# Kernel optimization log

Hardware: AMD Instinct MI355X
Metric: run time of the kernel (lower is better)

## Reference

```python
import jax, jax.numpy as jnp
import numpy as np

N_NODES = 10000
DEG = 32          # random neighbors per node; +1 self loop (A + I in original)
BATCH = 2
F_IN = 128
D_EMB = 128


def _make_edges():
    # np.where on a dense (A+I) matrix yields edges sorted by source row;
    # we build the same sorted-by-src edge list directly.
    rng = np.random.default_rng(0)
    src = np.repeat(np.arange(N_NODES), DEG + 1)
    dst = rng.integers(0, N_NODES, size=N_NODES * (DEG + 1))
    dst[DEG::DEG + 1] = np.arange(N_NODES)  # guarantee self loops
    return np.stack([src, dst], axis=1).astype(np.int32)  # [E, 2]


def setup_inputs() -> dict:
    key = jax.random.key(0)
    k1, k2, k3 = jax.random.split(key, 3)
    inputs = jax.random.normal(k1, (BATCH, N_NODES, F_IN), jnp.float32)
    W = jax.random.normal(k2, (F_IN, D_EMB), jnp.float32) * 0.1
    W_attn = jax.random.normal(k3, (2 * D_EMB, 1), jnp.float32) * 0.1
    edges = jnp.asarray(_make_edges())
    return {"inputs": inputs, "W": W, "W_attn": W_attn, "edges": edges}


def reference(inputs, W, W_attn, edges):
    # inputs: [B, N, F]; W: [F, D]; W_attn: [2D, 1]; edges: [E, 2] (sorted by src)
    B, N, _ = inputs.shape
    D = W.shape[1]
    src, dst = edges[:, 0], edges[:, 1]

    h = inputs @ W  # [B, N, D] node_states_transformed

    # Original: gather [src,dst] feats, reshape to [B,E,2D], matmul W_attn.
    # Equivalent efficient form: split W_attn and project per node first.
    a_src, a_dst = W_attn[:D, 0], W_attn[D:, 0]
    s = h @ a_src  # [B, N]
    d = h @ a_dst  # [B, N]
    scores = jax.nn.leaky_relu(s[:, src] + d[:, dst], negative_slope=0.2)  # [B, E]
    scores = jnp.exp(jnp.clip(scores, -2.0, 2.0))

    # Faithful to original bug: denominator uses batch 0 only, shared across batch.
    denom = jax.ops.segment_sum(scores[0], src, num_segments=N)  # [N]
    # edges sorted by src => tf.repeat(denom, bincount(src)) == denom[src]
    attn = scores / denom[src][None, :]  # [B, E]

    msgs = h[:, dst] * attn[:, :, None]  # [B, E, D]
    # tf.unsorted_segment_sum with rank-2 segment_ids sums over batch AND edges.
    out = jax.ops.segment_sum(msgs.sum(axis=0), src, num_segments=N)  # [N, D]
    return jnp.broadcast_to(out[None], (B, N, D))
```

## Files before the change

kernel.cpp:

```cpp
#include <hip/hip_runtime.h>
#include <math.h>

#define N_NODES 10000
#define DEG1 33
#define D_EMB 128
#define F_IN 128
#define BATCH 2

typedef short s8v  __attribute__((ext_vector_type(8)));
typedef float f4v  __attribute__((ext_vector_type(4)));

static __device__ __forceinline__ unsigned short f2bf(float f) {
    unsigned int x = __float_as_uint(f);
    unsigned int r = (x + 0x7fffu + ((x >> 16) & 1u)) >> 16;
    return (unsigned short)r;
}
static __device__ __forceinline__ float bf_lo(unsigned int u) { return __uint_as_float(u << 16); }
static __device__ __forceinline__ float bf_hi(unsigned int u) { return __uint_as_float(u & 0xffff0000u); }

__global__ __launch_bounds__(256) void gat_prep_kernel(
    const float* __restrict__ W, unsigned short* __restrict__ wtf)
{
    const int c = blockIdx.x;
    const int t = threadIdx.x;
    __shared__ float xs[128 * 16];
    #pragma unroll
    for (int r = 0; r < 8; ++r) {
        const int k = r * 16 + (t >> 4);
        const int n = t & 15;
        xs[k * 16 + n] = W[k * 128 + c * 16 + n];
    }
    __syncthreads();
    const int s = t >> 6;
    const int l = t & 63;
    s8v frag;
    #pragma unroll
    for (int j = 0; j < 8; ++j) {
        const int k = s * 32 + (l >> 4) * 8 + j;
        frag[j] = (short)f2bf(xs[k * 16 + (l & 15)]);
    }
    *(s8v*)&wtf[(((size_t)c * 4 + s) * 64 + l) * 8] = frag;
}

__global__ __launch_bounds__(256) void gat_h_kernel(
    const float* __restrict__ X, const unsigned short* __restrict__ wtf,
    const float* __restrict__ Wattn,
    unsigned short* __restrict__ hb, float* __restrict__ s_arr, float* __restrict__ d_arr)
{
    const int w = blockIdx.x * 4 + (threadIdx.x >> 6);
    if (w >= (BATCH * N_NODES) / 16) return;
    const int lane = threadIdx.x & 63;
    const int quad = lane >> 4;
    const int mrow = lane & 15;
    const int row0 = w * 16;

    f4v acc[8];
    #pragma unroll
    for (int c = 0; c < 8; ++c) acc[c] = (f4v){0.f, 0.f, 0.f, 0.f};

    const float* xrow = X + (size_t)(row0 + mrow) * F_IN;
    #pragma unroll
    for (int s = 0; s < 4; ++s) {
        const int k0 = s * 32 + quad * 8;
        const float4 xa = *(const float4*)&xrow[k0];
        const float4 xbv = *(const float4*)&xrow[k0 + 4];
        s8v a;
        a[0] = (short)f2bf(xa.x);  a[1] = (short)f2bf(xa.y);
        a[2] = (short)f2bf(xa.z);  a[3] = (short)f2bf(xa.w);
        a[4] = (short)f2bf(xbv.x); a[5] = (short)f2bf(xbv.y);
        a[6] = (short)f2bf(xbv.z); a[7] = (short)f2bf(xbv.w);
        #pragma unroll
        for (int c = 0; c < 8; ++c) {
            const s8v b = *(const s8v*)&wtf[(((size_t)c * 4 + s) * 64 + lane) * 8];
            acc[c] = __builtin_amdgcn_mfma_f32_16x16x32_bf16(a, b, acc[c], 0, 0, 0);
        }
    }

    const int b = (row0 >= N_NODES) ? 1 : 0;
    #pragma unroll
    for (int r = 0; r < 4; ++r) {
        const int R = row0 + quad * 4 + r;
        const int n = R - b * N_NODES;
        unsigned short* dst = &hb[((size_t)n * 2 + b) * D_EMB + mrow];
        #pragma unroll
        for (int c = 0; c < 8; ++c)
            dst[c * 16] = f2bf(acc[c][r]);
    }

    float as[8], ad[8];
    #pragma unroll
    for (int c = 0; c < 8; ++c) {
        as[c] = Wattn[c * 16 + mrow];
        ad[c] = Wattn[D_EMB + c * 16 + mrow];
    }
    #pragma unroll
    for (int r = 0; r < 4; ++r) {
        float sv = 0.f, dv = 0.f;
        #pragma unroll
        for (int c = 0; c < 8; ++c) {
            sv = fmaf(acc[c][r], as[c], sv);
            dv = fmaf(acc[c][r], ad[c], dv);
        }
        #pragma unroll
        for (int off = 1; off < 16; off <<= 1) {
            sv += __shfl_xor(sv, off, 16);
            dv += __shfl_xor(dv, off, 16);
        }
        if (mrow == 0) {
            const int R = row0 + quad * 4 + r;
            s_arr[R] = sv;
            d_arr[R] = dv;
        }
    }
}

__global__ __launch_bounds__(128) void gat_agg_kernel(
    const unsigned int* __restrict__ hb32, const float* __restrict__ s_arr,
    const float* __restrict__ d_arr, const int* __restrict__ edges,
    float* __restrict__ out)
{
    const int i = blockIdx.x;
    const int t = threadIdx.x;
    const int b = t >> 6;
    const int lane = t & 63;

    __shared__ int dsts[DEG1];
    __shared__ float scs[2][DEG1];
    __shared__ float inv_denom;
    __shared__ float red[2][2 * 64];

    float v = 0.f;
    if (lane < DEG1) {
        const int dst = edges[((size_t)i * DEG1 + lane) * 2 + 1];
        const float x0 = s_arr[b * N_NODES + i] + d_arr[b * N_NODES + dst];
        float x = (x0 >= 0.f) ? x0 : 0.2f * x0;
        x = fminf(fmaxf(x, -2.f), 2.f);
        const float sc = __expf(x);
        scs[b][lane] = sc;
        if (b == 0) { dsts[lane] = dst; v = sc; }
    }
    #pragma unroll
    for (int off = 32; off > 0; off >>= 1) v += __shfl_down(v, off, 64);
    if (t == 0) inv_denom = 1.f / v;
    __syncthreads();

    float ax = 0.f, ay = 0.f;
    #pragma unroll
    for (int j = 0; j < DEG1; ++j) {
        const int dd = dsts[j];
        const float wgt = scs[b][j];
        const unsigned int hv = hb32[((size_t)dd * 2 + b) * (D_EMB / 2) + lane];
        ax = fmaf(wgt, bf_lo(hv), ax);
        ay = fmaf(wgt, bf_hi(hv), ay);
    }
    red[b][2 * lane] = ax;
    red[b][2 * lane + 1] = ay;
    __syncthreads();

    const float inv = inv_denom;
    float2 o;
    o.x = (red[0][2 * lane] + red[1][2 * lane]) * inv;
    o.y = (red[0][2 * lane + 1] + red[1][2 * lane + 1]) * inv;
    *(float2*)&out[((size_t)b * N_NODES + i) * D_EMB + 2 * lane] = o;
}

extern "C" void kernel_launch(void* const* d_in, const int* in_sizes, int n_in,
                              void* d_out, int out_size, void* d_ws, size_t ws_size,
                              hipStream_t stream) {
    const float* X     = (const float*)d_in[0];
    const float* W     = (const float*)d_in[1];
    const float* Wattn = (const float*)d_in[2];
    const int*   edges = (const int*)d_in[3];
    float* out = (float*)d_out;

    unsigned short* wtf = (unsigned short*)d_ws;
    unsigned short* hb  = wtf + 16384;
    float* s_arr = (float*)(hb + (size_t)BATCH * N_NODES * D_EMB);
    float* d_arr = s_arr + BATCH * N_NODES;

    gat_prep_kernel<<<8, 256, 0, stream>>>(W, wtf);
    gat_h_kernel<<<313, 256, 0, stream>>>(X, wtf, Wattn, hb, s_arr, d_arr);
    gat_agg_kernel<<<N_NODES, 128, 0, stream>>>((const unsigned int*)hb, s_arr, d_arr, edges, out);
}
```

Before: 93.23 us.

## Split h GEMM columns across wave pairs and process nodes per wave in aggregation

The h projection kernel now gives each pair of waves one 16-row tile, with each wave computing half of the output columns. The partial attention dot products are combined through shared memory, which doubles the number of blocks for better occupancy. The aggregation kernel now gives one 64-lane wave per node and loops over 4 nodes per wave. It broadcasts neighbor indices and scores with shuffles instead of LDS and barriers, and gathers both batches with 8-byte loads. This removes per-node block launch and sync overhead, but each wave has less parallelism per node and the gathers are serialized across a longer per-wave loop.

```diff
diff --git a/kernel.cpp b/kernel.cpp
--- a/kernel.cpp
+++ b/kernel.cpp
@@ -47,16 +47,18 @@
     const float* __restrict__ Wattn,
     unsigned short* __restrict__ hb, float* __restrict__ s_arr, float* __restrict__ d_arr)
 {
-    const int w = blockIdx.x * 4 + (threadIdx.x >> 6);
-    if (w >= (BATCH * N_NODES) / 16) return;
+    __shared__ float lds_sd[2][2][2][16];
+    const int wave = threadIdx.x >> 6;
     const int lane = threadIdx.x & 63;
     const int quad = lane >> 4;
     const int mrow = lane & 15;
-    const int row0 = w * 16;
+    const int rg   = wave >> 1;
+    const int half = wave & 1;
+    const int row0 = (blockIdx.x * 2 + rg) * 16;
 
-    f4v acc[8];
+    f4v acc[4];
     #pragma unroll
-    for (int c = 0; c < 8; ++c) acc[c] = (f4v){0.f, 0.f, 0.f, 0.f};
+    for (int cc = 0; cc < 4; ++cc) acc[cc] = (f4v){0.f, 0.f, 0.f, 0.f};
 
     const float* xrow = X + (size_t)(row0 + mrow) * F_IN;
     #pragma unroll
@@ -70,9 +72,10 @@
         a[4] = (short)f2bf(xbv.x); a[5] = (short)f2bf(xbv.y);
         a[6] = (short)f2bf(xbv.z); a[7] = (short)f2bf(xbv.w);
         #pragma unroll
-        for (int c = 0; c < 8; ++c) {
+        for (int cc = 0; cc < 4; ++cc) {
+            const int c = half * 4 + cc;
             const s8v b = *(const s8v*)&wtf[(((size_t)c * 4 + s) * 64 + lane) * 8];
-            acc[c] = __builtin_amdgcn_mfma_f32_16x16x32_bf16(a, b, acc[c], 0, 0, 0);
+            acc[cc] = __builtin_amdgcn_mfma_f32_16x16x32_bf16(a, b, acc[cc], 0, 0, 0);
         }
     }
 
@@ -81,25 +84,25 @@
     for (int r = 0; r < 4; ++r) {
         const int R = row0 + quad * 4 + r;
         const int n = R - b * N_NODES;
-        unsigned short* dst = &hb[((size_t)n * 2 + b) * D_EMB + mrow];
+        unsigned short* dst = &hb[((size_t)n * 2 + b) * D_EMB + half * 64 + mrow];
         #pragma unroll
-        for (int c = 0; c < 8; ++c)
-            dst[c * 16] = f2bf(acc[c][r]);
+        for (int cc = 0; cc < 4; ++cc)
+            dst[cc * 16] = f2bf(acc[cc][r]);
     }
 
-    float as[8], ad[8];
+    float as[4], ad[4];
     #pragma unroll
-    for (int c = 0; c < 8; ++c) {
-        as[c] = Wattn[c * 16 + mrow];
-        ad[c] = Wattn[D_EMB + c * 16 + mrow];
+    for (int cc = 0; cc < 4; ++cc) {
+        as[cc] = Wattn[(half * 4 + cc) * 16 + mrow];
+        ad[cc] = Wattn[D_EMB + (half * 4 + cc) * 16 + mrow];
     }
     #pragma unroll
     for (int r = 0; r < 4; ++r) {
         float sv = 0.f, dv = 0.f;
         #pragma unroll
-        for (int c = 0; c < 8; ++c) {
-            sv = fmaf(acc[c][r], as[c], sv);
-            dv = fmaf(acc[c][r], ad[c], dv);
+        for (int cc = 0; cc < 4; ++cc) {
+            sv = fmaf(acc[cc][r], as[cc], sv);
+            dv = fmaf(acc[cc][r], ad[cc], dv);
         }
         #pragma unroll
         for (int off = 1; off < 16; off <<= 1) {
@@ -107,61 +110,72 @@
             dv += __shfl_xor(dv, off, 16);
         }
         if (mrow == 0) {
-            const int R = row0 + quad * 4 + r;
-            s_arr[R] = sv;
-            d_arr[R] = dv;
+            lds_sd[rg][half][0][quad * 4 + r] = sv;
+            lds_sd[rg][half][1][quad * 4 + r] = dv;
         }
+    }
+    __syncthreads();
+    const int t = threadIdx.x;
+    if (t < 64) {
+        const int rg2 = t >> 5, r = (t >> 1) & 15, which = t & 1;
+        const float val = lds_sd[rg2][0][which][r] + lds_sd[rg2][1][which][r];
+        const int row = (blockIdx.x * 2 + rg2) * 16 + r;
+        if (which == 0) s_arr[row] = val; else d_arr[row] = val;
     }
 }
 
-__global__ __launch_bounds__(128) void gat_agg_kernel(
-    const unsigned int* __restrict__ hb32, const float* __restrict__ s_arr,
+__global__ __launch_bounds__(256) void gat_agg_kernel(
+    const uint2* __restrict__ h2, const float* __restrict__ s_arr,
     const float* __restrict__ d_arr, const int* __restrict__ edges,
     float* __restrict__ out)
 {
-    const int i = blockIdx.x;
-    const int t = threadIdx.x;
-    const int b = t >> 6;
-    const int lane = t & 63;
+    const int wid  = blockIdx.x * 4 + (threadIdx.x >> 6);
+    const int lane = threadIdx.x & 63;
 
-    __shared__ int dsts[DEG1];
-    __shared__ float scs[2][DEG1];
-    __shared__ float inv_denom;
-    __shared__ float red[2][2 * 64];
+    for (int it = 0; it < 4; ++it) {
+        const int i = wid * 4 + it;
 
-    float v = 0.f;
-    if (lane < DEG1) {
-        const int dst = edges[((size_t)i * DEG1 + lane) * 2 + 1];
-        const float x0 = s_arr[b * N_NODES + i] + d_arr[b * N_NODES + dst];
-        float x = (x0 >= 0.f) ? x0 : 0.2f * x0;
-        x = fminf(fmaxf(x, -2.f), 2.f);
-        const float sc = __expf(x);
-        scs[b][lane] = sc;
-        if (b == 0) { dsts[lane] = dst; v = sc; }
+        int dstv = 0; float sc0 = 0.f, sc1 = 0.f;
+        if (lane < DEG1) {
+            dstv = edges[((size_t)i * DEG1 + lane) * 2 + 1];
+            float x0 = s_arr[i] + d_arr[dstv];
+            float x1 = s_arr[N_NODES + i] + d_arr[N_NODES + dstv];
+            x0 = (x0 >= 0.f) ? x0 : 0.2f * x0;
+            x1 = (x1 >= 0.f) ? x1 : 0.2f * x1;
+            x0 = fminf(fmaxf(x0, -2.f), 2.f);
+            x1 = fminf(fmaxf(x1, -2.f), 2.f);
+            sc0 = __expf(x0);
+            sc1 = __expf(x1);
+        }
+        float dsum = sc0;
+        #pragma unroll
+        for (int off = 1; off < 64; off <<= 1) dsum += __shfl_xor(dsum, off, 64);
+        const float inv = 1.f / dsum;
+
+        const float4 zero = make_float4(0.f, 0.f, 0.f, 0.f);
+        float4 acc = zero;
+        #pragma unroll
+        for (int j = 0; j < DEG1; ++j) {
+            const int   dd = __shfl(dstv, j, 64);
+            const float w0 = __shfl(sc0,  j, 64);
+            const float w1 = __shfl(sc1,  j, 64);
+            const float wgt = (lane < 32) ? w0 : w1;
+            const uint2 hv = h2[(size_t)dd * 64 + lane];
+            acc.x = fmaf(wgt, bf_lo(hv.x), acc.x);
+            acc.y = fmaf(wgt, bf_hi(hv.x), acc.y);
+            acc.z = fmaf(wgt, bf_lo(hv.y), acc.z);
+            acc.w = fmaf(wgt, bf_hi(hv.y), acc.w);
+        }
+        float4 o;
+        o.x = (acc.x + __shfl_xor(acc.x, 32, 64)) * inv;
+        o.y = (acc.y + __shfl_xor(acc.y, 32, 64)) * inv;
+        o.z = (acc.z + __shfl_xor(acc.z, 32, 64)) * inv;
+        o.w = (acc.w + __shfl_xor(acc.w, 32, 64)) * inv;
+
+        const int b  = lane >> 5;
+        const int dl = lane & 31;
+        *(float4*)&out[((size_t)b * N_NODES + i) * D_EMB + dl * 4] = o;
     }
-    #pragma unroll
-    for (int off = 32; off > 0; off >>= 1) v += __shfl_down(v, off, 64);
-    if (t == 0) inv_denom = 1.f / v;
-    __syncthreads();
-
-    float ax = 0.f, ay = 0.f;
-    #pragma unroll
-    for (int j = 0; j < DEG1; ++j) {
-        const int dd = dsts[j];
-        const float wgt = scs[b][j];
-        const unsigned int hv = hb32[((size_t)dd * 2 + b) * (D_EMB / 2) + lane];
-        ax = fmaf(wgt, bf_lo(hv), ax);
-        ay = fmaf(wgt, bf_hi(hv), ay);
-    }
-    red[b][2 * lane] = ax;
-    red[b][2 * lane + 1] = ay;
-    __syncthreads();
-
-    const float inv = inv_denom;
-    float2 o;
-    o.x = (red[0][2 * lane] + red[1][2 * lane]) * inv;
-    o.y = (red[0][2 * lane + 1] + red[1][2 * lane + 1]) * inv;
-    *(float2*)&out[((size_t)b * N_NODES + i) * D_EMB + 2 * lane] = o;
 }
 
 extern "C" void kernel_launch(void* const* d_in, const int* in_sizes, int n_in,
@@ -179,6 +193,6 @@
     float* d_arr = s_arr + BATCH * N_NODES;
 
     gat_prep_kernel<<<8, 256, 0, stream>>>(W, wtf);
-    gat_h_kernel<<<313, 256, 0, stream>>>(X, wtf, Wattn, hb, s_arr, d_arr);
-    gat_agg_kernel<<<N_NODES, 128, 0, stream>>>((const unsigned int*)hb, s_arr, d_arr, edges, out);
+    gat_h_kernel<<<625, 256, 0, stream>>>(X, wtf, Wattn, hb, s_arr, d_arr);
+    gat_agg_kernel<<<625, 256, 0, stream>>>((const uint2*)hb, s_arr, d_arr, edges, out);
 }
```

After: 100.8 us. +8.1%, slower.

## Use single-wave aggregation with readlane broadcasts instead of shared memory

Applied to the files above, without the earlier changes.

The aggregation kernel now runs one 64-lane wave per node instead of two waves. Edge destinations and scores stay in registers and are broadcast with readlane rather than staged through shared memory, which removes both __syncthreads. Each lane loads 8 bytes of the interleaved two-batch row: lanes 0-31 cover batch 0 and lanes 32-63 cover batch 1. A cross-half shuffle then produces the shared output, which is written as float4. This halves the thread count per block and removes LDS traffic, at the cost of doing the batch-1 score computation redundantly in the same wave.

```diff
diff --git a/kernel.cpp b/kernel.cpp
--- a/kernel.cpp
+++ b/kernel.cpp
@@ -17,6 +17,9 @@
 }
 static __device__ __forceinline__ float bf_lo(unsigned int u) { return __uint_as_float(u << 16); }
 static __device__ __forceinline__ float bf_hi(unsigned int u) { return __uint_as_float(u & 0xffff0000u); }
+static __device__ __forceinline__ float rdlane_f(float v, int l) {
+    return __uint_as_float((unsigned int)__builtin_amdgcn_readlane((int)__float_as_uint(v), l));
+}
 
 __global__ __launch_bounds__(256) void gat_prep_kernel(
     const float* __restrict__ W, unsigned short* __restrict__ wtf)
@@ -114,54 +117,53 @@
     }
 }
 
-__global__ __launch_bounds__(128) void gat_agg_kernel(
-    const unsigned int* __restrict__ hb32, const float* __restrict__ s_arr,
+__global__ __launch_bounds__(64) void gat_agg_kernel(
+    const uint2* __restrict__ h2, const float* __restrict__ s_arr,
     const float* __restrict__ d_arr, const int* __restrict__ edges,
     float* __restrict__ out)
 {
     const int i = blockIdx.x;
-    const int t = threadIdx.x;
-    const int b = t >> 6;
-    const int lane = t & 63;
+    const int lane = threadIdx.x;
 
-    __shared__ int dsts[DEG1];
-    __shared__ float scs[2][DEG1];
-    __shared__ float inv_denom;
-    __shared__ float red[2][2 * 64];
+    int dstv = 0; float sc0 = 0.f, sc1 = 0.f;
+    if (lane < DEG1) {
+        dstv = edges[((size_t)i * DEG1 + lane) * 2 + 1];
+        float x0 = s_arr[i] + d_arr[dstv];
+        float x1 = s_arr[N_NODES + i] + d_arr[N_NODES + dstv];
+        x0 = (x0 >= 0.f) ? x0 : 0.2f * x0;
+        x1 = (x1 >= 0.f) ? x1 : 0.2f * x1;
+        sc0 = __expf(fminf(fmaxf(x0, -2.f), 2.f));
+        sc1 = __expf(fminf(fmaxf(x1, -2.f), 2.f));
+    }
+    float dsum = sc0;
+    #pragma unroll
+    for (int off = 1; off < 64; off <<= 1) dsum += __shfl_xor(dsum, off, 64);
+    const float inv = 1.f / dsum;
+    sc0 *= inv;
+    sc1 *= inv;
 
-    float v = 0.f;
-    if (lane < DEG1) {
-        const int dst = edges[((size_t)i * DEG1 + lane) * 2 + 1];
-        const float x0 = s_arr[b * N_NODES + i] + d_arr[b * N_NODES + dst];
-        float x = (x0 >= 0.f) ? x0 : 0.2f * x0;
-        x = fminf(fmaxf(x, -2.f), 2.f);
-        const float sc = __expf(x);
-        scs[b][lane] = sc;
-        if (b == 0) { dsts[lane] = dst; v = sc; }
-    }
-    #pragma unroll
-    for (int off = 32; off > 0; off >>= 1) v += __shfl_down(v, off, 64);
-    if (t == 0) inv_denom = 1.f / v;
-    __syncthreads();
-
-    float ax = 0.f, ay = 0.f;
+    float4 acc = make_float4(0.f, 0.f, 0.f, 0.f);
     #pragma unroll
     for (int j = 0; j < DEG1; ++j) {
-        const int dd = dsts[j];
-        const float wgt = scs[b][j];
-        const unsigned int hv = hb32[((size_t)dd * 2 + b) * (D_EMB / 2) + lane];
-        ax = fmaf(wgt, bf_lo(hv), ax);
-        ay = fmaf(wgt, bf_hi(hv), ay);
+        const int   dd = __builtin_amdgcn_readlane(dstv, j);
+        const float w0 = rdlane_f(sc0, j);
+        const float w1 = rdlane_f(sc1, j);
+        const float wgt = (lane < 32) ? w0 : w1;
+        const uint2 hv = h2[(size_t)dd * 64 + lane];
+        acc.x = fmaf(wgt, bf_lo(hv.x), acc.x);
+        acc.y = fmaf(wgt, bf_hi(hv.x), acc.y);
+        acc.z = fmaf(wgt, bf_lo(hv.y), acc.z);
+        acc.w = fmaf(wgt, bf_hi(hv.y), acc.w);
     }
-    red[b][2 * lane] = ax;
-    red[b][2 * lane + 1] = ay;
-    __syncthreads();
+    float4 o;
+    o.x = acc.x + __shfl_xor(acc.x, 32, 64);
+    o.y = acc.y + __shfl_xor(acc.y, 32, 64);
+    o.z = acc.z + __shfl_xor(acc.z, 32, 64);
+    o.w = acc.w + __shfl_xor(acc.w, 32, 64);
 
-    const float inv = inv_denom;
-    float2 o;
-    o.x = (red[0][2 * lane] + red[1][2 * lane]) * inv;
-    o.y = (red[0][2 * lane + 1] + red[1][2 * lane + 1]) * inv;
-    *(float2*)&out[((size_t)b * N_NODES + i) * D_EMB + 2 * lane] = o;
+    const int b  = lane >> 5;
+    const int dl = lane & 31;
+    *(float4*)&out[((size_t)b * N_NODES + i) * D_EMB + dl * 4] = o;
 }
 
 extern "C" void kernel_launch(void* const* d_in, const int* in_sizes, int n_in,
@@ -180,5 +182,5 @@
 
     gat_prep_kernel<<<8, 256, 0, stream>>>(W, wtf);
     gat_h_kernel<<<313, 256, 0, stream>>>(X, wtf, Wattn, hb, s_arr, d_arr);
-    gat_agg_kernel<<<N_NODES, 128, 0, stream>>>((const unsigned int*)hb, s_arr, d_arr, edges, out);
+    gat_agg_kernel<<<N_NODES, 64, 0, stream>>>((const uint2*)hb, s_arr, d_arr, edges, out);
 }
```

Measured after the change: 91.17 us. -2.2%, faster.
